# Performance work log

Measured on AMD Instinct MI355X. Metric: run time of the kernel, lower is better.

The kernel has to match this reference:

```python
import jax, jax.numpy as jnp
import numpy as np

V, E, H, C, T = 50000, 512, 1024, 1221, 4096


def setup_inputs() -> dict:
    key = jax.random.key(0)
    ks = jax.random.split(key, 8)
    s = 1.0 / np.sqrt(H)  # PyTorch LSTM/Linear init scale
    return {
        "x": jax.random.randint(ks[0], (T,), 0, V),
        "emb_table": jax.random.normal(ks[1], (V, E), jnp.float32),
        "W_ih": jax.random.uniform(ks[2], (4 * H, 2 * E), jnp.float32, -s, s),
        "W_hh": jax.random.uniform(ks[3], (4 * H, H), jnp.float32, -s, s),
        "b_ih": jax.random.uniform(ks[4], (4 * H,), jnp.float32, -s, s),
        "b_hh": jax.random.uniform(ks[5], (4 * H,), jnp.float32, -s, s),
        "W_out": jax.random.uniform(ks[6], (C, H), jnp.float32, -s, s),
        "b_out": jax.random.uniform(ks[7], (C,), jnp.float32, -s, s),
    }


def reference(x, emb_table, W_ih, W_hh, b_ih, b_hh, W_out, b_out):
    emb = emb_table[x]                       # [T, E]
    last = emb[-1]                           # [E] embedding of final token
    n = emb.shape[0] - 1
    # each step input: concat(word_i, word_last) -> [T-1, 2E]
    xs = jnp.concatenate(
        [emb[:-1], jnp.broadcast_to(last, (n, last.shape[0]))], axis=1
    )
    # Precompute input projections for all steps in one GEMM: [T-1, 4H]
    x_gates = xs @ W_ih.T + b_ih + b_hh
    hdim = W_hh.shape[1]

    def step(carry, xg):
        h, c = carry
        gates = xg + h @ W_hh.T              # [4H], PyTorch gate order i,f,g,o
        i, f, g, o = jnp.split(gates, 4)
        i = jax.nn.sigmoid(i)
        f = jax.nn.sigmoid(f)
        g = jnp.tanh(g)
        o = jax.nn.sigmoid(o)
        c = f * c + i * g
        h = o * jnp.tanh(c)
        return (h, c), h

    h0 = jnp.zeros((hdim,), dtype=x_gates.dtype)
    c0 = jnp.zeros((hdim,), dtype=x_gates.dtype)
    _, hs = jax.lax.scan(step, (h0, c0), x_gates)  # hs: [T-1, H]
    out = hs @ W_out.T + b_out                     # [T-1, C]
    return out[None, :, :]                         # (1, T-1, C)
```

## Files before the change

### kernel.cpp

```cpp
#include <hip/hip_runtime.h>
#include <math.h>

#define NSTEP 4095
#define EDIM  512
#define HDIM  1024
#define GDIM  4096
#define KDIM  1024
#define CDIM  1221
#define SNWG  64
#define SNT   512
#define HPAD  36

#define PIN4(v) asm volatile("" : "+v"((v).x), "+v"((v).y), "+v"((v).z), "+v"((v).w))

__device__ __forceinline__ float sigmoidf_(float v) {
    return 1.0f / (1.0f + __expf(-v));
}
__device__ __forceinline__ float tanhf_(float v) {
    v = fminf(fmaxf(v, -15.0f), 15.0f);
    const float e2 = __expf(2.0f * v);
    return (e2 - 1.0f) / (e2 + 1.0f);
}

__global__ __launch_bounds__(256) void gemm_emb_kernel(
    const int* __restrict__ x, const float* __restrict__ emb,
    const float* __restrict__ W, const float* __restrict__ b_ih,
    const float* __restrict__ b_hh, float* __restrict__ xg)
{
    __shared__ float As[8][128];
    __shared__ float Bs[8][128];
    const int tid = threadIdx.x;
    const int bm = blockIdx.y * 128, bn = blockIdx.x * 128;
    const int tx = tid & 15, ty = tid >> 4;
    const int lrow = tid >> 1;
    const int lk4  = (tid & 1) * 4;
    const int lastTok = x[NSTEP];
    const int am = bm + lrow;
    const int tokRow = (am < NSTEP) ? x[am] : 0;
    const int bnrow = bn + lrow;

    float acc[8][8];
#pragma unroll
    for (int i = 0; i < 8; ++i)
#pragma unroll
        for (int j = 0; j < 8; ++j) acc[i][j] = 0.0f;

    for (int k0 = 0; k0 < KDIM; k0 += 8) {
        const int k = k0 + lk4;
        float4 av = make_float4(0.f, 0.f, 0.f, 0.f);
        if (am < NSTEP) {
            const int tok = (k < EDIM) ? tokRow : lastTok;
            const int kk  = (k < EDIM) ? k : (k - EDIM);
            av = *(const float4*)(emb + (size_t)tok * EDIM + kk);
        }
        const float4 bv = *(const float4*)(W + (size_t)bnrow * KDIM + k);
        __syncthreads();
        As[lk4 + 0][lrow] = av.x; As[lk4 + 1][lrow] = av.y;
        As[lk4 + 2][lrow] = av.z; As[lk4 + 3][lrow] = av.w;
        Bs[lk4 + 0][lrow] = bv.x; Bs[lk4 + 1][lrow] = bv.y;
        Bs[lk4 + 2][lrow] = bv.z; Bs[lk4 + 3][lrow] = bv.w;
        __syncthreads();
#pragma unroll
        for (int kk = 0; kk < 8; ++kk) {
            const float4 a0 = *(const float4*)&As[kk][ty * 4];
            const float4 a1 = *(const float4*)&As[kk][ty * 4 + 64];
            const float4 b0 = *(const float4*)&Bs[kk][tx * 4];
            const float4 b1 = *(const float4*)&Bs[kk][tx * 4 + 64];
            const float a[8] = {a0.x, a0.y, a0.z, a0.w, a1.x, a1.y, a1.z, a1.w};
            const float b[8] = {b0.x, b0.y, b0.z, b0.w, b1.x, b1.y, b1.z, b1.w};
#pragma unroll
            for (int i = 0; i < 8; ++i)
#pragma unroll
                for (int j = 0; j < 8; ++j) acc[i][j] += a[i] * b[j];
        }
    }
#pragma unroll
    for (int i = 0; i < 8; ++i) {
        const int m = bm + ((i < 4) ? (ty * 4 + i) : (64 + ty * 4 + i - 4));
        if (m >= NSTEP) continue;
#pragma unroll
        for (int j = 0; j < 8; ++j) {
            const int n = bn + ((j < 4) ? (tx * 4 + j) : (64 + tx * 4 + j - 4));
            xg[(size_t)m * GDIM + n] = acc[i][j] + b_ih[n] + b_hh[n];
        }
    }
}

__global__ __launch_bounds__(256) void gemm_out_kernel(
    const float* __restrict__ A, const float* __restrict__ W,
    const float* __restrict__ bias, float* __restrict__ C)
{
    __shared__ float As[8][128];
    __shared__ float Bs[8][128];
    const int tid = threadIdx.x;
    const int bm = blockIdx.y * 128, bn = blockIdx.x * 128;
    const int tx = tid & 15, ty = tid >> 4;
    const int lrow = tid >> 1;
    const int lk4  = (tid & 1) * 4;
    const int am = bm + lrow;
    const int bnrow = bn + lrow;

    float acc[8][8];
#pragma unroll
    for (int i = 0; i < 8; ++i)
#pragma unroll
        for (int j = 0; j < 8; ++j) acc[i][j] = 0.0f;

    for (int k0 = 0; k0 < KDIM; k0 += 8) {
        const int k = k0 + lk4;
        float4 av = make_float4(0.f, 0.f, 0.f, 0.f);
        if (am < NSTEP) av = *(const float4*)(A + (size_t)am * KDIM + k);
        float4 bv = make_float4(0.f, 0.f, 0.f, 0.f);
        if (bnrow < CDIM) bv = *(const float4*)(W + (size_t)bnrow * KDIM + k);
        __syncthreads();
        As[lk4 + 0][lrow] = av.x; As[lk4 + 1][lrow] = av.y;
        As[lk4 + 2][lrow] = av.z; As[lk4 + 3][lrow] = av.w;
        Bs[lk4 + 0][lrow] = bv.x; Bs[lk4 + 1][lrow] = bv.y;
        Bs[lk4 + 2][lrow] = bv.z; Bs[lk4 + 3][lrow] = bv.w;
        __syncthreads();
#pragma unroll
        for (int kk = 0; kk < 8; ++kk) {
            const float4 a0 = *(const float4*)&As[kk][ty * 4];
            const float4 a1 = *(const float4*)&As[kk][ty * 4 + 64];
            const float4 b0 = *(const float4*)&Bs[kk][tx * 4];
            const float4 b1 = *(const float4*)&Bs[kk][tx * 4 + 64];
            const float a[8] = {a0.x, a0.y, a0.z, a0.w, a1.x, a1.y, a1.z, a1.w};
            const float b[8] = {b0.x, b0.y, b0.z, b0.w, b1.x, b1.y, b1.z, b1.w};
#pragma unroll
            for (int i = 0; i < 8; ++i)
#pragma unroll
                for (int j = 0; j < 8; ++j) acc[i][j] += a[i] * b[j];
        }
    }
#pragma unroll
    for (int i = 0; i < 8; ++i) {
        const int m = bm + ((i < 4) ? (ty * 4 + i) : (64 + ty * 4 + i - 4));
        if (m >= NSTEP) continue;
#pragma unroll
        for (int j = 0; j < 8; ++j) {
            const int n = bn + ((j < 4) ? (tx * 4 + j) : (64 + tx * 4 + j - 4));
            if (n < CDIM) C[(size_t)m * CDIM + n] = acc[i][j] + bias[n];
        }
    }
}

__global__ __launch_bounds__(512, 2) void scan_kernel(
    const float* __restrict__ xg, const float* __restrict__ Whh,
    float* __restrict__ hs, unsigned long long* hb)
{
    __shared__ float h_s[2][32 * HPAD];
    const int tid  = threadIdx.x;
    const int u    = tid >> 5;
    const int s    = tid & 31;
    const int unit = blockIdx.x * 16 + u;

    float4 w4[4][8];
#pragma unroll
    for (int q = 0; q < 4; ++q)
#pragma unroll
        for (int jj = 0; jj < 8; ++jj)
            w4[q][jj] = *(const float4*)(
                Whh + (size_t)(q * HDIM + unit) * KDIM + s * 32 + jj * 4);

    for (int i = tid; i < 2 * 32 * HPAD; i += SNT) ((float*)h_s)[i] = 0.0f;
    __syncthreads();

    float c = 0.0f;
    const int sbase = s * HPAD;

    for (int t = 1; t <= NSTEP; ++t) {
#pragma unroll
        for (int q = 0; q < 4; ++q) {
            PIN4(w4[q][0]); PIN4(w4[q][1]); PIN4(w4[q][2]); PIN4(w4[q][3]);
            PIN4(w4[q][4]); PIN4(w4[q][5]); PIN4(w4[q][6]); PIN4(w4[q][7]);
        }

        const int par = (t - 1) & 1;

        float xgv = 0.0f;
        if (s < 4) xgv = xg[(size_t)(t - 1) * GDIM + s * HDIM + unit];

        if (t > 1) {
            const int want = t - 1;
            const unsigned long long* p = hb + (size_t)par * HDIM + tid;
            unsigned long long v0 = 0, v1 = 0;
            unsigned pend = 0x3u;
            do {
                if (pend & 1u) v0 = __hip_atomic_load(p,       __ATOMIC_RELAXED, __HIP_MEMORY_SCOPE_AGENT);
                if (pend & 2u) v1 = __hip_atomic_load(p + 512, __ATOMIC_RELAXED, __HIP_MEMORY_SCOPE_AGENT);
                if ((pend & 1u) && (int)(v0 >> 32) == want) pend &= ~1u;
                if ((pend & 2u) && (int)(v1 >> 32) == want) pend &= ~2u;
            } while (pend);
            h_s[par][u * HPAD + s]        = __uint_as_float((unsigned)v0);
            h_s[par][(u + 16) * HPAD + s] = __uint_as_float((unsigned)v1);
        }
        __syncthreads();

        float a0 = 0.0f, a1 = 0.0f, a2 = 0.0f, a3 = 0.0f;
#pragma unroll
        for (int jj = 0; jj < 8; ++jj) {
            const float4 h4 = *(const float4*)&h_s[par][sbase + jj * 4];
            a0 += w4[0][jj].x * h4.x + w4[0][jj].y * h4.y + w4[0][jj].z * h4.z + w4[0][jj].w * h4.w;
            a1 += w4[1][jj].x * h4.x + w4[1][jj].y * h4.y + w4[1][jj].z * h4.z + w4[1][jj].w * h4.w;
            a2 += w4[2][jj].x * h4.x + w4[2][jj].y * h4.y + w4[2][jj].z * h4.z + w4[2][jj].w * h4.w;
            a3 += w4[3][jj].x * h4.x + w4[3][jj].y * h4.y + w4[3][jj].z * h4.z + w4[3][jj].w * h4.w;
        }
        a0 += (s == 0) ? xgv : 0.0f;
        a1 += (s == 1) ? xgv : 0.0f;
        a2 += (s == 2) ? xgv : 0.0f;
        a3 += (s == 3) ? xgv : 0.0f;
#pragma unroll
        for (int m = 1; m < 32; m <<= 1) {
            a0 += __shfl_xor(a0, m, 64);
            a1 += __shfl_xor(a1, m, 64);
            a2 += __shfl_xor(a2, m, 64);
            a3 += __shfl_xor(a3, m, 64);
        }

        const float ig = sigmoidf_(a0);
        const float fg = sigmoidf_(a1);
        const float gg = tanhf_(a2);
        const float og = sigmoidf_(a3);
        c = fg * c + ig * gg;
        const float h = og * tanhf_(c);

        if (s == 0) {
            hs[(size_t)(t - 1) * HDIM + unit] = h;
            const unsigned long long pv =
                ((unsigned long long)(unsigned)t << 32) | __float_as_uint(h);
            __hip_atomic_store(&hb[(size_t)(t & 1) * HDIM + unit], pv,
                               __ATOMIC_RELAXED, __HIP_MEMORY_SCOPE_AGENT);
        }
    }
}

extern "C" void kernel_launch(void* const* d_in, const int* in_sizes, int n_in,
                              void* d_out, int out_size, void* d_ws, size_t ws_size,
                              hipStream_t stream)
{
    const int*   x     = (const int*)d_in[0];
    const float* emb   = (const float*)d_in[1];
    const float* W_ih  = (const float*)d_in[2];
    const float* W_hh  = (const float*)d_in[3];
    const float* b_ih  = (const float*)d_in[4];
    const float* b_hh  = (const float*)d_in[5];
    const float* W_out = (const float*)d_in[6];
    const float* b_out = (const float*)d_in[7];
    float* out = (float*)d_out;

    float* xg = (float*)d_ws;
    float* hs = xg + (size_t)NSTEP * GDIM;
    unsigned long long* hb =
        (unsigned long long*)(hs + (size_t)NSTEP * HDIM);

    dim3 blk(256);
    dim3 g1(GDIM / 128, 32);
    gemm_emb_kernel<<<g1, blk, 0, stream>>>(x, emb, W_ih, b_ih, b_hh, xg);

    scan_kernel<<<dim3(SNWG), dim3(SNT), 0, stream>>>(xg, W_hh, hs, hb);

    dim3 g2((CDIM + 127) / 128, 32);
    gemm_out_kernel<<<g2, blk, 0, stream>>>(hs, W_out, b_out, out);
}
```

Baseline: 9.870 ms.

## Widen scan workgroups to 1024 threads with one wavefront per hidden unit

The recurrent scan kernel moves from 512 threads (half a wavefront per unit, 32 K-elements per lane) to 1024 threads (a full 64-lane wavefront per unit, 16 K-elements per lane). Each thread now holds half as many W_hh registers and polls only one flag word instead of two. The reduction gains one more shuffle stage, and the shared h layout is re-padded to fit the new mapping. The aim is shorter per-step dependency chains and fewer registers, in exchange for larger workgroups and a costlier __syncthreads barrier.

After: 15.30 ms. +55.0%, slower.

```diff
diff --git a/kernel.cpp b/kernel.cpp
--- a/kernel.cpp
+++ b/kernel.cpp
@@ -8,8 +8,8 @@
 #define KDIM  1024
 #define CDIM  1221
 #define SNWG  64
-#define SNT   512
-#define HPAD  36
+#define SNT   1024
+#define HSPAD 20
 
 #define PIN4(v) asm volatile("" : "+v"((v).x), "+v"((v).y), "+v"((v).z), "+v"((v).w))
 
@@ -144,73 +144,68 @@
     }
 }
 
-__global__ __launch_bounds__(512, 2) void scan_kernel(
+__global__ __launch_bounds__(1024, 4) void scan_kernel(
     const float* __restrict__ xg, const float* __restrict__ Whh,
     float* __restrict__ hs, unsigned long long* hb)
 {
-    __shared__ float h_s[2][32 * HPAD];
+    __shared__ float h_s[2][64 * HSPAD];
     const int tid  = threadIdx.x;
-    const int u    = tid >> 5;
-    const int s    = tid & 31;
-    const int unit = blockIdx.x * 16 + u;
-
-    float4 w4[4][8];
+    const int wv   = tid >> 6;
+    const int lane = tid & 63;
+    const int unit = blockIdx.x * 16 + wv;
+
+    float4 w4[4][4];
 #pragma unroll
     for (int q = 0; q < 4; ++q)
 #pragma unroll
-        for (int jj = 0; jj < 8; ++jj)
+        for (int jj = 0; jj < 4; ++jj)
             w4[q][jj] = *(const float4*)(
-                Whh + (size_t)(q * HDIM + unit) * KDIM + s * 32 + jj * 4);
-
-    for (int i = tid; i < 2 * 32 * HPAD; i += SNT) ((float*)h_s)[i] = 0.0f;
+                Whh + (size_t)(q * HDIM + unit) * KDIM + lane * 16 + jj * 4);
+
+    for (int i = tid; i < 2 * 64 * HSPAD; i += SNT) ((float*)h_s)[i] = 0.0f;
     __syncthreads();
 
     float c = 0.0f;
-    const int sbase = s * HPAD;
+    const int sbase = lane * HSPAD;
 
     for (int t = 1; t <= NSTEP; ++t) {
 #pragma unroll
         for (int q = 0; q < 4; ++q) {
             PIN4(w4[q][0]); PIN4(w4[q][1]); PIN4(w4[q][2]); PIN4(w4[q][3]);
-            PIN4(w4[q][4]); PIN4(w4[q][5]); PIN4(w4[q][6]); PIN4(w4[q][7]);
         }
 
         const int par = (t - 1) & 1;
 
         float xgv = 0.0f;
-        if (s < 4) xgv = xg[(size_t)(t - 1) * GDIM + s * HDIM + unit];
+        if (lane < 4) xgv = xg[(size_t)(t - 1) * GDIM + lane * HDIM + unit];
 
         if (t > 1) {
             const int want = t - 1;
             const unsigned long long* p = hb + (size_t)par * HDIM + tid;
-            unsigned long long v0 = 0, v1 = 0;
-            unsigned pend = 0x3u;
-            do {
-                if (pend & 1u) v0 = __hip_atomic_load(p,       __ATOMIC_RELAXED, __HIP_MEMORY_SCOPE_AGENT);
-                if (pend & 2u) v1 = __hip_atomic_load(p + 512, __ATOMIC_RELAXED, __HIP_MEMORY_SCOPE_AGENT);
-                if ((pend & 1u) && (int)(v0 >> 32) == want) pend &= ~1u;
-                if ((pend & 2u) && (int)(v1 >> 32) == want) pend &= ~2u;
-            } while (pend);
-            h_s[par][u * HPAD + s]        = __uint_as_float((unsigned)v0);
-            h_s[par][(u + 16) * HPAD + s] = __uint_as_float((unsigned)v1);
+            unsigned long long v0;
+            for (;;) {
+                v0 = __hip_atomic_load(p, __ATOMIC_RELAXED, __HIP_MEMORY_SCOPE_AGENT);
+                if ((int)(v0 >> 32) == want) break;
+            }
+            h_s[par][(tid >> 4) * HSPAD + (tid & 15)] = __uint_as_float((unsigned)v0);
         }
         __syncthreads();
 
         float a0 = 0.0f, a1 = 0.0f, a2 = 0.0f, a3 = 0.0f;
 #pragma unroll
-        for (int jj = 0; jj < 8; ++jj) {
+        for (int jj = 0; jj < 4; ++jj) {
             const float4 h4 = *(const float4*)&h_s[par][sbase + jj * 4];
             a0 += w4[0][jj].x * h4.x + w4[0][jj].y * h4.y + w4[0][jj].z * h4.z + w4[0][jj].w * h4.w;
             a1 += w4[1][jj].x * h4.x + w4[1][jj].y * h4.y + w4[1][jj].z * h4.z + w4[1][jj].w * h4.w;
             a2 += w4[2][jj].x * h4.x + w4[2][jj].y * h4.y + w4[2][jj].z * h4.z + w4[2][jj].w * h4.w;
             a3 += w4[3][jj].x * h4.x + w4[3][jj].y * h4.y + w4[3][jj].z * h4.z + w4[3][jj].w * h4.w;
         }
-        a0 += (s == 0) ? xgv : 0.0f;
-        a1 += (s == 1) ? xgv : 0.0f;
-        a2 += (s == 2) ? xgv : 0.0f;
-        a3 += (s == 3) ? xgv : 0.0f;
-#pragma unroll
-        for (int m = 1; m < 32; m <<= 1) {
+        a0 += (lane == 0) ? xgv : 0.0f;
+        a1 += (lane == 1) ? xgv : 0.0f;
+        a2 += (lane == 2) ? xgv : 0.0f;
+        a3 += (lane == 3) ? xgv : 0.0f;
+#pragma unroll
+        for (int m = 1; m < 64; m <<= 1) {
             a0 += __shfl_xor(a0, m, 64);
             a1 += __shfl_xor(a1, m, 64);
             a2 += __shfl_xor(a2, m, 64);
@@ -224,7 +219,7 @@
         c = fg * c + ig * gg;
         const float h = og * tanhf_(c);
 
-        if (s == 0) {
+        if (lane == 0) {
             hs[(size_t)(t - 1) * HDIM + unit] = h;
             const unsigned long long pv =
                 ((unsigned long long)(unsigned)t << 32) | __float_as_uint(h);
```
